# Kernel tuning notes

Hardware: AMD Instinct MI355X
Metric: run time of the kernel (lower is better)

Reference implementation:

```python
import jax, jax.numpy as jnp
import numpy as np
import math

B, C, H, W = 2, 64, 64, 64
DI = 2 * C          # d_inner
N = 16              # d_state
R = math.ceil(C / 16)  # dt_rank
K = 3               # d_conv
L = H * W

PARAM_KEYS = [
    'pe_x_w', 'pe_x_b', 'rms_x_w', 'conv_x_w', 'conv_x_b',
    'pe_info_w', 'pe_info_b', 'rms_info_w', 'conv_info_w', 'conv_info_b',
    'pe_mask_w', 'pe_mask_b', 'rms_mask_w', 'conv_mask_w', 'conv_mask_b',
    'in_x_w', 'in_info_w', 'in_mask_w',
    'delta_w', 'dt_w', 'dt_b', 'B_w', 'C_w', 'A_log', 'out_w',
]


def setup_inputs():
    key = jax.random.key(0)
    ki = iter(jax.random.split(key, 40))
    def nrm(shape, scale=1.0):
        return jax.random.normal(next(ki), shape, jnp.float32) * scale
    sc, sdi, sr, sk = 1/np.sqrt(C), 1/np.sqrt(DI), 1/np.sqrt(R), 1/np.sqrt(K)
    inp = {}
    for name in ('up', 'mask', 'x', 'y', 'z'):
        inp[name] = nrm((B, C, H, W))
    for role in ('x', 'info', 'mask'):
        inp[f'pe_{role}_w'] = nrm((3, C, C), sc)
        inp[f'pe_{role}_b'] = jnp.zeros((3, C), jnp.float32)
        inp[f'rms_{role}_w'] = jnp.ones((3, C), jnp.float32)
        inp[f'conv_{role}_w'] = nrm((3, DI, K), sk)
        inp[f'conv_{role}_b'] = nrm((3, DI), sk)
    inp['in_x_w'] = nrm((3, 2 * DI, C), sc)
    inp['in_info_w'] = nrm((3, DI, C), sc)
    inp['in_mask_w'] = nrm((3, DI, C), sc)
    inp['delta_w'] = nrm((3, R, DI), sdi)
    inp['dt_w'] = nrm((3, DI, R), sr)
    rng = np.random.default_rng(0)
    dt = np.exp(rng.uniform(size=(3, DI)) * (np.log(0.1) - np.log(0.001)) + np.log(0.001)).clip(min=1e-4)
    inp['dt_b'] = jnp.asarray(np.log(-np.expm1(-dt)), jnp.float32)
    inp['B_w'] = nrm((3, N, DI), sdi)
    inp['C_w'] = nrm((3, N, DI), sdi)
    inp['A_log'] = jnp.tile(jnp.log(jnp.arange(1, N + 1, dtype=jnp.float32)), (3, DI, 1))
    inp['out_w'] = nrm((3, C, DI), sdi)
    return inp


def embed1x1(t, w, b):
    # PatchEmbed with patch_size=1: 1x1 conv then flatten to [B, L, C]
    y = jnp.einsum('bchw,oc->bohw', t, w) + b[None, :, None, None]
    bb, cc, hh, ww = y.shape
    return y.reshape(bb, cc, hh * ww).transpose(0, 2, 1)


def rms_norm(x, w, eps=1e-5):
    return x * jax.lax.rsqrt(jnp.mean(x * x, axis=-1, keepdims=True) + eps) * w


def causal_dwconv_silu(x, w, b):
    # x [B, D, L]; depthwise causal conv1d (left-pad K-1), then SiLU
    kk = w.shape[1]
    xp = jnp.pad(x, ((0, 0), (0, 0), (kk - 1, 0)))
    y = jax.lax.conv_general_dilated(
        xp, w[:, None, :], window_strides=(1,), padding='VALID',
        dimension_numbers=('NCH', 'OIH', 'NCH'), feature_group_count=w.shape[0])
    return jax.nn.silu(y + b[None, :, None])


def selective_scan(u, delta, A, Bm, Cm):
    # u, delta: [B, D, L]; A: [D, N]; Bm, Cm: [B, N, L]
    dA = jnp.exp(jnp.einsum('bdl,dn->lbdn', delta, A))           # [L,B,D,N]
    dBu = jnp.einsum('bdl,bnl,bdl->lbdn', delta, Bm, u)          # [L,B,D,N]
    Ct = Cm.transpose(2, 0, 1)                                   # [L,B,N]
    h0 = jnp.zeros((u.shape[0], u.shape[1], A.shape[1]), u.dtype)
    def step(h, inp):
        dA_t, dBu_t, C_t = inp
        h = dA_t * h + dBu_t
        return h, jnp.einsum('bdn,bn->bd', h, C_t)
    _, ys = jax.lax.scan(step, h0, (dA, dBu, Ct))
    return ys.transpose(1, 2, 0)                                 # [B,D,L]


def branch(xin, maskin, upin, p):
    bb, cc, hh, ww = xin.shape
    xe = rms_norm(embed1x1(xin, p['pe_x_w'], p['pe_x_b']), p['rms_x_w'])        # [B,L,C]
    xz = jnp.einsum('blc,dc->bdl', xe, p['in_x_w'])                              # [B,2DI,L]
    di = xz.shape[1] // 2
    xc, x_act = xz[:, :di], xz[:, di:]
    info = rms_norm(embed1x1(upin, p['pe_info_w'], p['pe_info_b']), p['rms_info_w'])
    info = jnp.einsum('blc,dc->bdl', info, p['in_info_w'])
    mk = rms_norm(embed1x1(maskin, p['pe_mask_w'], p['pe_mask_b']), p['rms_mask_w'])
    mk = jnp.einsum('blc,dc->bdl', mk, p['in_mask_w'])
    xc = causal_dwconv_silu(xc, p['conv_x_w'], p['conv_x_b'])
    mk = causal_dwconv_silu(mk, p['conv_mask_w'], p['conv_mask_b'])
    info = causal_dwconv_silu(info, p['conv_info_w'], p['conv_info_b'])
    # S6: delta from mask, B from info, C from x
    delta = jnp.einsum('bdl,rd->brl', mk, p['delta_w'])
    delta = jnp.einsum('brl,dr->bdl', delta, p['dt_w'])
    delta = jax.nn.softplus(delta + p['dt_b'][None, :, None])
    A = -jnp.exp(p['A_log'])
    Bm = jnp.einsum('bdl,nd->bnl', info, p['B_w'])
    Cm = jnp.einsum('bdl,nd->bnl', xc, p['C_w'])
    y = selective_scan(xc, delta, A, Bm, Cm)
    y = y * jax.nn.silu(x_act)
    y = jnp.einsum('bdl,cd->blc', y, p['out_w'])
    return y.transpose(0, 2, 1).reshape(bb, cc, hh, ww) + xin


def forward(up, mask, x, y, z, *params):
    pall = dict(zip(PARAM_KEYS, params))
    out = None
    for i, feat in enumerate((x, y, z)):
        p = {k: v[i] for k, v in pall.items()}
        o = branch(feat, mask, up, p)
        out = o if out is None else out + o
    return out


def reference(up, mask, x, y, z,
              pe_x_w, pe_x_b, rms_x_w, conv_x_w, conv_x_b,
              pe_info_w, pe_info_b, rms_info_w, conv_info_w, conv_info_b,
              pe_mask_w, pe_mask_b, rms_mask_w, conv_mask_w, conv_mask_b,
              in_x_w, in_info_w, in_mask_w,
              delta_w, dt_w, dt_b, B_w, C_w, A_log, out_w):
    return forward(up, mask, x, y, z,
                   pe_x_w, pe_x_b, rms_x_w, conv_x_w, conv_x_b,
                   pe_info_w, pe_info_b, rms_info_w, conv_info_w, conv_info_b,
                   pe_mask_w, pe_mask_b, rms_mask_w, conv_mask_w, conv_mask_b,
                   in_x_w, in_info_w, in_mask_w,
                   delta_w, dt_w, dt_b, B_w, C_w, A_log, out_w)
```

## Files before the change

### kernel.cpp

```cpp
#include <hip/hip_runtime.h>
#include <math.h>

namespace {

constexpr int NB = 3;
constexpr int BB = 2;
constexpr int CC = 64;
constexpr int LLEN = 4096;
constexpr int DI = 128;
constexpr int NN = 16;
constexpr int RR = 4;
constexpr int GG = 256;
constexpr int LC = 16;
constexpr int NSEQ = NB * BB * DI * NN;
constexpr size_t SBUF = (size_t)NB * BB * DI * LLEN;

typedef _Float16 f16;
typedef __attribute__((ext_vector_type(4))) float f32x4;
typedef __attribute__((ext_vector_type(8))) short bf16x8;
typedef __attribute__((ext_vector_type(4))) _Float16 f16x4;
typedef __attribute__((ext_vector_type(8))) _Float16 f16x8;

__device__ __forceinline__ float siluf(float v) { return v / (1.f + __expf(-v)); }

__device__ __forceinline__ short cvt_bf16(float f) {
    union { float f; unsigned u; } v; v.f = f;
    unsigned r = v.u + 0x7fffu + ((v.u >> 16) & 1u);
    return (short)(r >> 16);
}
__device__ __forceinline__ unsigned pack_bf16(float lo, float hi) {
    return ((unsigned)(unsigned short)cvt_bf16(hi) << 16) | (unsigned short)cvt_bf16(lo);
}
__device__ __forceinline__ bf16x8 pack8(float4 a, float4 b) {
    bf16x8 r;
    r[0] = cvt_bf16(a.x); r[1] = cvt_bf16(a.y); r[2] = cvt_bf16(a.z); r[3] = cvt_bf16(a.w);
    r[4] = cvt_bf16(b.x); r[5] = cvt_bf16(b.y); r[6] = cvt_bf16(b.z); r[7] = cvt_bf16(b.w);
    return r;
}
__device__ __forceinline__ f16x4 to_h4(float a, float b, float c, float d) {
    f16x4 r; r[0] = (f16)a; r[1] = (f16)b; r[2] = (f16)c; r[3] = (f16)d; return r;
}
__device__ __forceinline__ float4 to_f4(f16x4 v) {
    return make_float4((float)v[0], (float)v[1], (float)v[2], (float)v[3]);
}

__global__ __launch_bounds__(256) void k1_embed(
    const float* __restrict__ up, const float* __restrict__ mask_,
    const float* __restrict__ fx, const float* __restrict__ fy, const float* __restrict__ fz,
    const float* __restrict__ pe_x_w, const float* __restrict__ pe_x_b, const float* __restrict__ rms_x_w,
    const float* __restrict__ pe_i_w, const float* __restrict__ pe_i_b, const float* __restrict__ rms_i_w,
    const float* __restrict__ pe_m_w, const float* __restrict__ pe_m_b, const float* __restrict__ rms_m_w,
    const float* __restrict__ in_x_w, const float* __restrict__ in_i_w, const float* __restrict__ in_m_w,
    f16* __restrict__ xc_pre, f16* __restrict__ x_act,
    f16* __restrict__ info_pre, f16* __restrict__ mk_pre)
{
    __shared__ short sE[64 * 64];
    __shared__ float red[4][64];
    __shared__ float sscl[64];

    int lt = blockIdx.x, job = blockIdx.y, b = blockIdx.z;
    int i = job / 3, r = job % 3;
    const float *src, *pw, *pb, *rw, *iw;
    if (r == 0) {
        src = (i == 0 ? fx : (i == 1 ? fy : fz));
        pw = pe_x_w + i * 4096; pb = pe_x_b + i * 64; rw = rms_x_w + i * 64;
        iw = in_x_w + (size_t)i * 256 * 64;
    } else if (r == 1) {
        src = up;
        pw = pe_i_w + i * 4096; pb = pe_i_b + i * 64; rw = rms_i_w + i * 64;
        iw = in_i_w + (size_t)i * 128 * 64;
    } else {
        src = mask_;
        pw = pe_m_w + i * 4096; pb = pe_m_b + i * 64; rw = rms_m_w + i * 64;
        iw = in_m_w + (size_t)i * 128 * 64;
    }
    int t = threadIdx.x;
    int w = t >> 6, lane = t & 63, lo = lane & 15, hi = lane >> 4;
    int l0 = lt * 64;
    const float* Xg = src + (size_t)b * 64 * LLEN;

    f32x4 acc1[4];
    #pragma unroll
    for (int nt = 0; nt < 4; ++nt) acc1[nt] = (f32x4){0.f, 0.f, 0.f, 0.f};

    #pragma unroll
    for (int ks = 0; ks < 2; ++ks) {
        const float* ap = pw + (16 * w + lo) * 64 + ks * 32 + hi * 8;
        bf16x8 a1 = pack8(*(const float4*)ap, *(const float4*)(ap + 4));
        #pragma unroll
        for (int nt = 0; nt < 4; ++nt) {
            const float* xc = Xg + (size_t)(ks * 32 + hi * 8) * LLEN + l0 + nt * 16 + lo;
            bf16x8 b1;
            #pragma unroll
            for (int j = 0; j < 8; ++j) b1[j] = cvt_bf16(xc[(size_t)j * LLEN]);
            acc1[nt] = __builtin_amdgcn_mfma_f32_16x16x32_bf16(a1, b1, acc1[nt], 0, 0, 0);
        }
    }

    float4 pbv = *(const float4*)&pb[16 * w + 4 * hi];
    float e_[4][4];
    #pragma unroll
    for (int nt = 0; nt < 4; ++nt) {
        e_[nt][0] = acc1[nt][0] + pbv.x;
        e_[nt][1] = acc1[nt][1] + pbv.y;
        e_[nt][2] = acc1[nt][2] + pbv.z;
        e_[nt][3] = acc1[nt][3] + pbv.w;
        float s = e_[nt][0] * e_[nt][0] + e_[nt][1] * e_[nt][1]
                + e_[nt][2] * e_[nt][2] + e_[nt][3] * e_[nt][3];
        s += __shfl_xor(s, 16);
        s += __shfl_xor(s, 32);
        if (lane < 16) red[w][nt * 16 + lo] = s;
    }
    __syncthreads();
    if (t < 64) {
        float s = red[0][t] + red[1][t] + red[2][t] + red[3][t];
        sscl[t] = rsqrtf(s * (1.f / 64.f) + 1e-5f);
    }
    __syncthreads();

    {
        int ob = 2 * w + (hi >> 1);
        #pragma unroll
        for (int nt = 0; nt < 4; ++nt) {
            float sc = sscl[16 * nt + lo];
            unsigned p0 = pack_bf16(e_[nt][0] * sc, e_[nt][1] * sc);
            unsigned p1 = pack_bf16(e_[nt][2] * sc, e_[nt][3] * sc);
            unsigned* p = (unsigned*)&sE[(16 * nt + lo) * 64 + (ob ^ (lo & 7)) * 8 + 4 * (hi & 1)];
            p[0] = p0; p[1] = p1;
        }
    }
    __syncthreads();

    bf16x8 b2[4][2];
    #pragma unroll
    for (int nt = 0; nt < 4; ++nt)
        #pragma unroll
        for (int ks = 0; ks < 2; ++ks) {
            int db = ks * 4 + hi;
            b2[nt][ks] = *(const bf16x8*)&sE[(16 * nt + lo) * 64 + (db ^ (lo & 7)) * 8];
        }

    size_t obase = ((size_t)(i * 2 + b)) * DI * LLEN;
    int MT = (r == 0) ? 4 : 2;
    for (int mm = 0; mm < MT; ++mm) {
        int m = MT * w + mm;
        bf16x8 a2[2];
        #pragma unroll
        for (int ks = 0; ks < 2; ++ks) {
            const float* wp = iw + (size_t)(16 * m + lo) * 64 + ks * 32 + hi * 8;
            float4 w0 = *(const float4*)wp;
            float4 w1 = *(const float4*)(wp + 4);
            float4 r0 = *(const float4*)&rw[ks * 32 + hi * 8];
            float4 r1 = *(const float4*)&rw[ks * 32 + hi * 8 + 4];
            w0.x *= r0.x; w0.y *= r0.y; w0.z *= r0.z; w0.w *= r0.w;
            w1.x *= r1.x; w1.y *= r1.y; w1.z *= r1.z; w1.w *= r1.w;
            a2[ks] = pack8(w0, w1);
        }
        f32x4 acc2[4];
        #pragma unroll
        for (int nt = 0; nt < 4; ++nt) acc2[nt] = (f32x4){0.f, 0.f, 0.f, 0.f};
        #pragma unroll
        for (int ks = 0; ks < 2; ++ks)
            #pragma unroll
            for (int nt = 0; nt < 4; ++nt)
                acc2[nt] = __builtin_amdgcn_mfma_f32_16x16x32_bf16(a2[ks], b2[nt][ks], acc2[nt], 0, 0, 0);

        int d0 = 16 * m + 4 * hi;
        f16* dst; int dd = d0;
        if (r == 0) { if (d0 < 128) dst = xc_pre; else { dst = x_act; dd = d0 - 128; } }
        else if (r == 1) dst = info_pre;
        else dst = mk_pre;
        #pragma unroll
        for (int nt = 0; nt < 4; ++nt) {
            int l = l0 + 16 * nt + lo;
            *(f16x4*)&dst[obase + (size_t)l * DI + dd] =
                to_h4(acc2[nt][0], acc2[nt][1], acc2[nt][2], acc2[nt][3]);
        }
    }
}

__global__ __launch_bounds__(256) void k3_conv(
    const f16* __restrict__ xc_pre, const f16* __restrict__ info_pre, const f16* __restrict__ mk_pre,
    const float* __restrict__ conv_x_w, const float* __restrict__ conv_x_b,
    const float* __restrict__ conv_i_w, const float* __restrict__ conv_i_b,
    const float* __restrict__ conv_m_w, const float* __restrict__ conv_m_b,
    const float* __restrict__ delta_w, const float* __restrict__ dt_w, const float* __restrict__ dt_b,
    const float* __restrict__ B_w, const float* __restrict__ C_w,
    f16* __restrict__ u, f16* __restrict__ delta,
    f16* __restrict__ Bm, f16* __restrict__ Cm)
{
    __shared__ __align__(16) float ot[64 * 128];
    __shared__ float rvec[4 * 64];

    int lt = blockIdx.x, ib = blockIdx.y, strm = blockIdx.z;
    int i = ib >> 1;
    int t = threadIdx.x;
    int l0 = lt * 64;
    size_t base = (size_t)ib * DI * LLEN;

    const f16 *inb; const float *cw, *cb;
    if (strm == 0)      { inb = mk_pre;   cw = conv_m_w + i * DI * 3; cb = conv_m_b + i * DI; }
    else if (strm == 1) { inb = info_pre; cw = conv_i_w + i * DI * 3; cb = conv_i_b + i * DI; }
    else                { inb = xc_pre;   cw = conv_x_w + i * DI * 3; cb = conv_x_b + i * DI; }

    {
        int d4 = t & 31, lq = t >> 5;
        int d = d4 * 4;
        float cw0[4], cw1[4], cw2[4], cbb[4];
        #pragma unroll
        for (int j = 0; j < 4; ++j) {
            cw0[j] = cw[(d + j) * 3 + 0];
            cw1[j] = cw[(d + j) * 3 + 1];
            cw2[j] = cw[(d + j) * 3 + 2];
            cbb[j] = cb[d + j];
        }
        int gl0 = l0 + lq * 8;
        float4 x0 = make_float4(0.f, 0.f, 0.f, 0.f), x1 = x0;
        if (gl0 >= 2) x0 = to_f4(*(const f16x4*)&inb[base + (size_t)(gl0 - 2) * DI + d]);
        if (gl0 >= 1) x1 = to_f4(*(const f16x4*)&inb[base + (size_t)(gl0 - 1) * DI + d]);
        #pragma unroll
        for (int li = 0; li < 8; ++li) {
            int l = lq * 8 + li;
            float4 x2 = to_f4(*(const f16x4*)&inb[base + (size_t)(gl0 + li) * DI + d]);
            float4 v;
            v.x = siluf(cw0[0] * x0.x + cw1[0] * x1.x + cw2[0] * x2.x + cbb[0]);
            v.y = siluf(cw0[1] * x0.y + cw1[1] * x1.y + cw2[1] * x2.y + cbb[1]);
            v.z = siluf(cw0[2] * x0.z + cw1[2] * x1.z + cw2[2] * x2.z + cbb[2]);
            v.w = siluf(cw0[3] * x0.w + cw1[3] * x1.w + cw2[3] * x2.w + cbb[3]);
            *(float4*)&ot[l * 128 + ((d4 * 4) ^ ((l & 7) << 2))] = v;
            if (strm == 2) *(f16x4*)&u[base + (size_t)(gl0 + li) * DI + d] = to_h4(v.x, v.y, v.z, v.w);
            x0 = x1; x1 = x2;
        }
    }
    __syncthreads();

    if (strm == 0) {
        {
            int l = t & 63, r = t >> 6, sw = (l & 7) << 2;
            const float* dw = delta_w + i * RR * DI + r * DI;
            float acc = 0.f;
            #pragma unroll
            for (int d4 = 0; d4 < 32; ++d4) {
                float4 v = *(const float4*)&ot[l * 128 + ((d4 * 4) ^ sw)];
                int db = d4 * 4;
                acc += dw[db] * v.x + dw[db + 1] * v.y + dw[db + 2] * v.z + dw[db + 3] * v.w;
            }
            rvec[r * 64 + l] = acc;
        }
        __syncthreads();
        {
            int d = t & 127, lh = t >> 7;
            const float* dtw = dt_w + i * DI * RR + d * RR;
            float w0 = dtw[0], w1 = dtw[1], w2 = dtw[2], w3 = dtw[3];
            float bb = dt_b[i * DI + d];
            #pragma unroll 4
            for (int li = 0; li < 32; ++li) {
                int l = lh * 32 + li;
                float v = bb + w0 * rvec[l] + w1 * rvec[64 + l] + w2 * rvec[128 + l] + w3 * rvec[192 + l];
                float sp = (v > 20.f) ? v : log1pf(__expf(v));
                delta[base + (size_t)(l0 + l) * DI + d] = (f16)sp;
            }
        }
    } else {
        int l = t & 63, ng = t >> 6, sw = (l & 7) << 2;
        const float* wv = ((strm == 1) ? B_w : C_w) + i * NN * DI + ng * 4 * DI;
        float a0 = 0.f, a1 = 0.f, a2 = 0.f, a3 = 0.f;
        #pragma unroll
        for (int d4 = 0; d4 < 32; ++d4) {
            float4 v = *(const float4*)&ot[l * 128 + ((d4 * 4) ^ sw)];
            int db = d4 * 4;
            a0 += wv[db] * v.x + wv[db + 1] * v.y + wv[db + 2] * v.z + wv[db + 3] * v.w;
            a1 += wv[DI + db] * v.x + wv[DI + db + 1] * v.y + wv[DI + db + 2] * v.z + wv[DI + db + 3] * v.w;
            a2 += wv[2 * DI + db] * v.x + wv[2 * DI + db + 1] * v.y + wv[2 * DI + db + 2] * v.z + wv[2 * DI + db + 3] * v.w;
            a3 += wv[3 * DI + db] * v.x + wv[3 * DI + db + 1] * v.y + wv[3 * DI + db + 2] * v.z + wv[3 * DI + db + 3] * v.w;
        }
        f16* dst = (strm == 1) ? Bm : Cm;
        *(f16x4*)&dst[((size_t)ib * LLEN + l0 + l) * NN + ng * 4] = to_h4(a0, a1, a2, a3);
    }
}

__global__ __launch_bounds__(128) void k4_scan1(
    const f16* __restrict__ u, const f16* __restrict__ delta,
    const f16* __restrict__ Bm, const float* __restrict__ A_log,
    f16* __restrict__ aprod, f16* __restrict__ hend)
{
    __shared__ __align__(16) float sB[LC * 16];
    int g = blockIdx.x, ib = blockIdx.y, i = ib >> 1;
    int d = threadIdx.x;
    if (d < 64) {
        f16x4 v = ((const f16x4*)(Bm + ((size_t)ib * LLEN + (size_t)g * LC) * NN))[d];
        ((float4*)sB)[d] = to_f4(v);
    }
    float A[16], h[16];
    {
        const float4* al = (const float4*)(A_log + ((size_t)i * DI + d) * NN);
        #pragma unroll
        for (int q = 0; q < 4; ++q) {
            float4 v = al[q];
            A[4 * q] = -__expf(v.x); A[4 * q + 1] = -__expf(v.y);
            A[4 * q + 2] = -__expf(v.z); A[4 * q + 3] = -__expf(v.w);
        }
    }
    #pragma unroll
    for (int n = 0; n < 16; ++n) h[n] = 0.f;
    float sdl = 0.f;
    __syncthreads();
    size_t base = ((size_t)ib * LLEN + (size_t)g * LC) * DI + d;
    #pragma unroll 4
    for (int li = 0; li < LC; ++li) {
        float dl = (float)delta[base + li * DI];
        float du = dl * (float)u[base + li * DI];
        sdl += dl;
        const float4* bl = (const float4*)(sB + li * 16);
        float4 b0 = bl[0], b1 = bl[1], b2 = bl[2], b3 = bl[3];
        h[0] = __expf(dl * A[0]) * h[0] + du * b0.x;  h[1] = __expf(dl * A[1]) * h[1] + du * b0.y;
        h[2] = __expf(dl * A[2]) * h[2] + du * b0.z;  h[3] = __expf(dl * A[3]) * h[3] + du * b0.w;
        h[4] = __expf(dl * A[4]) * h[4] + du * b1.x;  h[5] = __expf(dl * A[5]) * h[5] + du * b1.y;
        h[6] = __expf(dl * A[6]) * h[6] + du * b1.z;  h[7] = __expf(dl * A[7]) * h[7] + du * b1.w;
        h[8] = __expf(dl * A[8]) * h[8] + du * b2.x;  h[9] = __expf(dl * A[9]) * h[9] + du * b2.y;
        h[10] = __expf(dl * A[10]) * h[10] + du * b2.z; h[11] = __expf(dl * A[11]) * h[11] + du * b2.w;
        h[12] = __expf(dl * A[12]) * h[12] + du * b3.x; h[13] = __expf(dl * A[13]) * h[13] + du * b3.y;
        h[14] = __expf(dl * A[14]) * h[14] + du * b3.z; h[15] = __expf(dl * A[15]) * h[15] + du * b3.w;
    }
    size_t seq = ((size_t)ib * DI + d) * NN;
    f16x8* ap = (f16x8*)(aprod + (size_t)g * NSEQ + seq);
    f16x8* he = (f16x8*)(hend + (size_t)g * NSEQ + seq);
    #pragma unroll
    for (int q = 0; q < 2; ++q) {
        f16x8 av, hv;
        #pragma unroll
        for (int j = 0; j < 8; ++j) {
            av[j] = (f16)__expf(A[8 * q + j] * sdl);
            hv[j] = (f16)h[8 * q + j];
        }
        ap[q] = av; he[q] = hv;
    }
}

__global__ __launch_bounds__(256) void k5_prefix(
    const f16* __restrict__ aprod, const f16* __restrict__ hend,
    f16* __restrict__ hin)
{
    int s = blockIdx.x * 256 + threadIdx.x;
    float h = 0.f;
    #pragma unroll 8
    for (int g = 0; g < GG; ++g) {
        hin[(size_t)g * NSEQ + s] = (f16)h;
        h = (float)aprod[(size_t)g * NSEQ + s] * h + (float)hend[(size_t)g * NSEQ + s];
    }
}

__global__ __launch_bounds__(128) void k6_scan2(
    const f16* __restrict__ u, const f16* __restrict__ delta,
    const f16* __restrict__ Bm, const f16* __restrict__ Cm,
    const float* __restrict__ A_log, const f16* __restrict__ hin,
    f16* __restrict__ y)
{
    __shared__ __align__(16) float sB[LC * 16];
    __shared__ __align__(16) float sC[LC * 16];
    int g = blockIdx.x, ib = blockIdx.y, i = ib >> 1;
    int d = threadIdx.x;
    {
        const f16x4* bsrc = (const f16x4*)(Bm + ((size_t)ib * LLEN + (size_t)g * LC) * NN);
        const f16x4* csrc = (const f16x4*)(Cm + ((size_t)ib * LLEN + (size_t)g * LC) * NN);
        if (d < 64) ((float4*)sB)[d] = to_f4(bsrc[d]);
        else ((float4*)sC)[d - 64] = to_f4(csrc[d - 64]);
    }
    float A[16], h[16];
    {
        const float4* al = (const float4*)(A_log + ((size_t)i * DI + d) * NN);
        #pragma unroll
        for (int q = 0; q < 4; ++q) {
            float4 v = al[q];
            A[4 * q] = -__expf(v.x); A[4 * q + 1] = -__expf(v.y);
            A[4 * q + 2] = -__expf(v.z); A[4 * q + 3] = -__expf(v.w);
        }
    }
    {
        size_t seq = ((size_t)ib * DI + d) * NN;
        const f16x8* hp = (const f16x8*)(hin + (size_t)g * NSEQ + seq);
        #pragma unroll
        for (int q = 0; q < 2; ++q) {
            f16x8 v = hp[q];
            #pragma unroll
            for (int j = 0; j < 8; ++j) h[8 * q + j] = (float)v[j];
        }
    }
    __syncthreads();
    size_t base = ((size_t)ib * LLEN + (size_t)g * LC) * DI + d;
    #pragma unroll 4
    for (int li = 0; li < LC; ++li) {
        float dl = (float)delta[base + li * DI];
        float du = dl * (float)u[base + li * DI];
        const float4* bl = (const float4*)(sB + li * 16);
        const float4* cl = (const float4*)(sC + li * 16);
        float4 b0 = bl[0], b1 = bl[1], b2 = bl[2], b3 = bl[3];
        float4 c0 = cl[0], c1 = cl[1], c2 = cl[2], c3 = cl[3];
        float acc = 0.f;
        h[0] = __expf(dl * A[0]) * h[0] + du * b0.x;  acc += h[0] * c0.x;
        h[1] = __expf(dl * A[1]) * h[1] + du * b0.y;  acc += h[1] * c0.y;
        h[2] = __expf(dl * A[2]) * h[2] + du * b0.z;  acc += h[2] * c0.z;
        h[3] = __expf(dl * A[3]) * h[3] + du * b0.w;  acc += h[3] * c0.w;
        h[4] = __expf(dl * A[4]) * h[4] + du * b1.x;  acc += h[4] * c1.x;
        h[5] = __expf(dl * A[5]) * h[5] + du * b1.y;  acc += h[5] * c1.y;
        h[6] = __expf(dl * A[6]) * h[6] + du * b1.z;  acc += h[6] * c1.z;
        h[7] = __expf(dl * A[7]) * h[7] + du * b1.w;  acc += h[7] * c1.w;
        h[8] = __expf(dl * A[8]) * h[8] + du * b2.x;  acc += h[8] * c2.x;
        h[9] = __expf(dl * A[9]) * h[9] + du * b2.y;  acc += h[9] * c2.y;
        h[10] = __expf(dl * A[10]) * h[10] + du * b2.z; acc += h[10] * c2.z;
        h[11] = __expf(dl * A[11]) * h[11] + du * b2.w; acc += h[11] * c2.w;
        h[12] = __expf(dl * A[12]) * h[12] + du * b3.x; acc += h[12] * c3.x;
        h[13] = __expf(dl * A[13]) * h[13] + du * b3.y; acc += h[13] * c3.y;
        h[14] = __expf(dl * A[14]) * h[14] + du * b3.z; acc += h[14] * c3.z;
        h[15] = __expf(dl * A[15]) * h[15] + du * b3.w; acc += h[15] * c3.w;
        y[base + li * DI] = (f16)acc;
    }
}

__global__ __launch_bounds__(256) void k7_out(
    const f16* __restrict__ y, const f16* __restrict__ xact,
    const float* __restrict__ out_w,
    const float* __restrict__ fx, const float* __restrict__ fy, const float* __restrict__ fz,
    float* __restrict__ out)
{
    __shared__ short sG[64 * 128];
    int lt = blockIdx.x, b = blockIdx.y;
    int l0 = lt * 64;
    int t = threadIdx.x;
    int w = t >> 6, lane = t & 63, lo = lane & 15, hi = lane >> 4;

    f32x4 acc[4];
    #pragma unroll
    for (int nt = 0; nt < 4; ++nt) acc[nt] = (f32x4){0.f, 0.f, 0.f, 0.f};

    for (int i = 0; i < 3; ++i) {
        size_t base = ((size_t)(i * 2 + b)) * DI * LLEN;
        __syncthreads();
        #pragma unroll
        for (int p = 0; p < 8; ++p) {
            int idx = t + 256 * p;
            int d4 = idx & 31, l = idx >> 5;
            int d = d4 * 4;
            float4 yv = to_f4(*(const f16x4*)&y[base + (size_t)(l0 + l) * DI + d]);
            float4 xa = to_f4(*(const f16x4*)&xact[base + (size_t)(l0 + l) * DI + d]);
            float g0 = yv.x * siluf(xa.x), g1 = yv.y * siluf(xa.y);
            float g2 = yv.z * siluf(xa.z), g3 = yv.w * siluf(xa.w);
            int blk = d4 >> 1;
            int blks = (blk & 8) | ((blk ^ (l & 7)) & 7);
            unsigned* p32 = (unsigned*)&sG[l * 128 + blks * 8 + 4 * (d4 & 1)];
            p32[0] = pack_bf16(g0, g1);
            p32[1] = pack_bf16(g2, g3);
        }
        __syncthreads();

        const float* ow = out_w + (size_t)i * CC * DI;
        bf16x8 a[4];
        #pragma unroll
        for (int ks = 0; ks < 4; ++ks) {
            const float* ap = ow + (size_t)(16 * w + lo) * 128 + ks * 32 + hi * 8;
            a[ks] = pack8(*(const float4*)ap, *(const float4*)(ap + 4));
        }
        #pragma unroll
        for (int nt = 0; nt < 4; ++nt) {
            int l = 16 * nt + lo;
            #pragma unroll
            for (int ks = 0; ks < 4; ++ks) {
                int db = ks * 4 + hi;
                int blks = (db & 8) | ((db ^ (l & 7)) & 7);
                bf16x8 bv = *(const bf16x8*)&sG[l * 128 + blks * 8];
                acc[nt] = __builtin_amdgcn_mfma_f32_16x16x32_bf16(a[ks], bv, acc[nt], 0, 0, 0);
            }
        }
    }

    #pragma unroll
    for (int nt = 0; nt < 4; ++nt) {
        int l = l0 + 16 * nt + lo;
        int cbase = 16 * w + 4 * hi;
        #pragma unroll
        for (int rr = 0; rr < 4; ++rr) {
            int c = cbase + rr;
            size_t idx = ((size_t)b * CC + c) * LLEN + l;
            out[idx] = acc[nt][rr] + fx[idx] + fy[idx] + fz[idx];
        }
    }
}

}

extern "C" void kernel_launch(void* const* d_in, const int* in_sizes, int n_in,
                              void* d_out, int out_size, void* d_ws, size_t ws_size,
                              hipStream_t stream)
{
    (void)in_sizes; (void)n_in; (void)out_size; (void)ws_size;
    const float* up       = (const float*)d_in[0];
    const float* mask_    = (const float*)d_in[1];
    const float* fx       = (const float*)d_in[2];
    const float* fy       = (const float*)d_in[3];
    const float* fz       = (const float*)d_in[4];
    const float* pe_x_w   = (const float*)d_in[5];
    const float* pe_x_b   = (const float*)d_in[6];
    const float* rms_x_w  = (const float*)d_in[7];
    const float* conv_x_w = (const float*)d_in[8];
    const float* conv_x_b = (const float*)d_in[9];
    const float* pe_i_w   = (const float*)d_in[10];
    const float* pe_i_b   = (const float*)d_in[11];
    const float* rms_i_w  = (const float*)d_in[12];
    const float* conv_i_w = (const float*)d_in[13];
    const float* conv_i_b = (const float*)d_in[14];
    const float* pe_m_w   = (const float*)d_in[15];
    const float* pe_m_b   = (const float*)d_in[16];
    const float* rms_m_w  = (const float*)d_in[17];
    const float* conv_m_w = (const float*)d_in[18];
    const float* conv_m_b = (const float*)d_in[19];
    const float* in_x_w   = (const float*)d_in[20];
    const float* in_i_w   = (const float*)d_in[21];
    const float* in_m_w   = (const float*)d_in[22];
    const float* delta_w  = (const float*)d_in[23];
    const float* dt_w     = (const float*)d_in[24];
    const float* dt_b     = (const float*)d_in[25];
    const float* B_w      = (const float*)d_in[26];
    const float* C_w      = (const float*)d_in[27];
    const float* A_log    = (const float*)d_in[28];
    const float* out_w    = (const float*)d_in[29];
    float* out = (float*)d_out;

    f16* ws = (f16*)d_ws;
    const size_t S = SBUF;
    f16* xc_pre   = ws;
    f16* x_act    = ws + S;
    f16* info_pre = ws + 2 * S;
    f16* mk_pre   = ws + 3 * S;
    f16* ubuf     = ws + 4 * S;
    f16* dbuf     = ws + 5 * S;
    f16* BmB      = ws + 6 * S;
    f16* CmB      = BmB + (size_t)NB * BB * NN * LLEN;
    f16* aprod = info_pre;
    f16* hendb = mk_pre;
    f16* hinb  = xc_pre;
    f16* ybuf  = info_pre;

    hipLaunchKernelGGL(k1_embed, dim3(64, 9, 2), dim3(256), 0, stream,
        up, mask_, fx, fy, fz,
        pe_x_w, pe_x_b, rms_x_w, pe_i_w, pe_i_b, rms_i_w, pe_m_w, pe_m_b, rms_m_w,
        in_x_w, in_i_w, in_m_w, xc_pre, x_act, info_pre, mk_pre);

    hipLaunchKernelGGL(k3_conv, dim3(64, 6, 3), dim3(256), 0, stream,
        xc_pre, info_pre, mk_pre,
        conv_x_w, conv_x_b, conv_i_w, conv_i_b, conv_m_w, conv_m_b,
        delta_w, dt_w, dt_b, B_w, C_w, ubuf, dbuf, BmB, CmB);

    hipLaunchKernelGGL(k4_scan1, dim3(GG, 6), dim3(128), 0, stream,
        ubuf, dbuf, BmB, A_log, aprod, hendb);

    hipLaunchKernelGGL(k5_prefix, dim3(NSEQ / 256), dim3(256), 0, stream,
        aprod, hendb, hinb);

    hipLaunchKernelGGL(k6_scan2, dim3(GG, 6), dim3(128), 0, stream,
        ubuf, dbuf, BmB, CmB, A_log, hinb, ybuf);

    hipLaunchKernelGGL(k7_out, dim3(64, 2), dim3(256), 0, stream,
        ybuf, x_act, out_w, fx, fy, fz, out);
}
```

Measured before the change: 133.0 us.

## Fuse conv, projections and first scan pass; move gating into second scan

The three-stream conv kernel becomes one kernel per chunk. It computes the mask, info and x convolutions in sequence and keeps the results in f16 shared memory. It then runs the chunk-local first scan pass in place, so the separate scan1 kernel and its reloads of u, delta and Bm are gone. The chunk count is halved and the chunk length doubled. The second scan now applies the SiLU(x_act) gate and writes bf16 directly, so the output kernel just copies tiles into shared memory. In exchange each fused block does more serial work, there are fewer blocks, and aprod/hend need extra workspace beyond the previous buffers.

Result: slower. 146.1 us (+9.8%).

```diff
diff --git a/kernel.cpp b/kernel.cpp
--- a/kernel.cpp
+++ b/kernel.cpp
@@ -10,8 +10,8 @@
 constexpr int DI = 128;
 constexpr int NN = 16;
 constexpr int RR = 4;
-constexpr int GG = 256;
-constexpr int LC = 16;
+constexpr int GG = 128;
+constexpr int LC = 32;
 constexpr int NSEQ = NB * BB * DI * NN;
 constexpr size_t SBUF = (size_t)NB * BB * DI * LLEN;
 
@@ -42,6 +42,11 @@
 }
 __device__ __forceinline__ float4 to_f4(f16x4 v) {
     return make_float4((float)v[0], (float)v[1], (float)v[2], (float)v[3]);
+}
+__device__ __forceinline__ int swz16(int l, int d) {
+    int b = d >> 3;
+    int bs = (b & 8) | ((b ^ l) & 7);
+    return l * 128 + bs * 8 + (d & 7);
 }
 
 __global__ __launch_bounds__(256) void k1_embed(
@@ -186,24 +191,25 @@
     const float* __restrict__ conv_m_w, const float* __restrict__ conv_m_b,
     const float* __restrict__ delta_w, const float* __restrict__ dt_w, const float* __restrict__ dt_b,
     const float* __restrict__ B_w, const float* __restrict__ C_w,
+    const float* __restrict__ A_log,
     f16* __restrict__ u, f16* __restrict__ delta,
-    f16* __restrict__ Bm, f16* __restrict__ Cm)
+    f16* __restrict__ Bm, f16* __restrict__ Cm,
+    f16* __restrict__ aprod, f16* __restrict__ hend)
 {
-    __shared__ __align__(16) float ot[64 * 128];
-    __shared__ float rvec[4 * 64];
-
-    int lt = blockIdx.x, ib = blockIdx.y, strm = blockIdx.z;
+    __shared__ __align__(16) f16 ot[LC * 128];
+    __shared__ __align__(16) f16 sdelH[LC * 128];
+    __shared__ __align__(16) f16 otU[LC * 128];
+    __shared__ __align__(16) float sB[LC * 16];
+    __shared__ float rvec[4 * LC];
+
+    int g = blockIdx.x, ib = blockIdx.y;
     int i = ib >> 1;
-    int t = threadIdx.x;
-    int l0 = lt * 64;
+    int t = threadIdx.x, lane = t & 63;
+    int l0 = g * LC;
     size_t base = (size_t)ib * DI * LLEN;
 
-    const f16 *inb; const float *cw, *cb;
-    if (strm == 0)      { inb = mk_pre;   cw = conv_m_w + i * DI * 3; cb = conv_m_b + i * DI; }
-    else if (strm == 1) { inb = info_pre; cw = conv_i_w + i * DI * 3; cb = conv_i_b + i * DI; }
-    else                { inb = xc_pre;   cw = conv_x_w + i * DI * 3; cb = conv_x_b + i * DI; }
-
-    {
+    auto conv_stream = [&](const f16* inb, const float* cw, const float* cb,
+                           f16* lds, bool store_u) {
         int d4 = t & 31, lq = t >> 5;
         int d = d4 * 4;
         float cw0[4], cw1[4], cw2[4], cbb[4];
@@ -214,126 +220,146 @@
             cw2[j] = cw[(d + j) * 3 + 2];
             cbb[j] = cb[d + j];
         }
-        int gl0 = l0 + lq * 8;
+        int gl0 = l0 + lq * 4;
         float4 x0 = make_float4(0.f, 0.f, 0.f, 0.f), x1 = x0;
         if (gl0 >= 2) x0 = to_f4(*(const f16x4*)&inb[base + (size_t)(gl0 - 2) * DI + d]);
         if (gl0 >= 1) x1 = to_f4(*(const f16x4*)&inb[base + (size_t)(gl0 - 1) * DI + d]);
         #pragma unroll
-        for (int li = 0; li < 8; ++li) {
-            int l = lq * 8 + li;
+        for (int li = 0; li < 4; ++li) {
+            int l = lq * 4 + li;
             float4 x2 = to_f4(*(const f16x4*)&inb[base + (size_t)(gl0 + li) * DI + d]);
             float4 v;
             v.x = siluf(cw0[0] * x0.x + cw1[0] * x1.x + cw2[0] * x2.x + cbb[0]);
             v.y = siluf(cw0[1] * x0.y + cw1[1] * x1.y + cw2[1] * x2.y + cbb[1]);
             v.z = siluf(cw0[2] * x0.z + cw1[2] * x1.z + cw2[2] * x2.z + cbb[2]);
             v.w = siluf(cw0[3] * x0.w + cw1[3] * x1.w + cw2[3] * x2.w + cbb[3]);
-            *(float4*)&ot[l * 128 + ((d4 * 4) ^ ((l & 7) << 2))] = v;
-            if (strm == 2) *(f16x4*)&u[base + (size_t)(gl0 + li) * DI + d] = to_h4(v.x, v.y, v.z, v.w);
+            f16x4 hv = to_h4(v.x, v.y, v.z, v.w);
+            *(f16x4*)&lds[swz16(l, d)] = hv;
+            if (store_u) *(f16x4*)&u[base + (size_t)(gl0 + li) * DI + d] = hv;
             x0 = x1; x1 = x2;
         }
-    }
-    __syncthreads();
-
-    if (strm == 0) {
-        {
-            int l = t & 63, r = t >> 6, sw = (l & 7) << 2;
-            const float* dw = delta_w + i * RR * DI + r * DI;
-            float acc = 0.f;
+    };
+
+    conv_stream(mk_pre, conv_m_w + i * DI * 3, conv_m_b + i * DI, ot, false);
+    __syncthreads();
+    {
+        int l = t & 31, r = t >> 6;
+        const float* dw = delta_w + i * RR * DI + r * DI;
+        float acc = 0.f;
+        #pragma unroll
+        for (int db = 0; db < 16; ++db) {
+            f16x8 v = *(const f16x8*)&ot[swz16(l, db * 8)];
+            int d0 = db * 8;
+            acc += dw[d0] * (float)v[0] + dw[d0 + 1] * (float)v[1]
+                 + dw[d0 + 2] * (float)v[2] + dw[d0 + 3] * (float)v[3]
+                 + dw[d0 + 4] * (float)v[4] + dw[d0 + 5] * (float)v[5]
+                 + dw[d0 + 6] * (float)v[6] + dw[d0 + 7] * (float)v[7];
+        }
+        if (lane < 32) rvec[r * LC + l] = acc;
+    }
+    __syncthreads();
+    {
+        int d = t & 127, lh = t >> 7;
+        const float* dtw = dt_w + i * DI * RR + d * RR;
+        float w0 = dtw[0], w1 = dtw[1], w2 = dtw[2], w3 = dtw[3];
+        float bb = dt_b[i * DI + d];
+        #pragma unroll
+        for (int li = 0; li < 16; ++li) {
+            int l = lh * 16 + li;
+            float v = bb + w0 * rvec[l] + w1 * rvec[LC + l] + w2 * rvec[2 * LC + l] + w3 * rvec[3 * LC + l];
+            float sp = (v > 20.f) ? v : log1pf(__expf(v));
+            f16 h = (f16)sp;
+            delta[base + (size_t)(l0 + l) * DI + d] = h;
+            sdelH[swz16(l, d)] = h;
+        }
+    }
+    __syncthreads();
+    conv_stream(info_pre, conv_i_w + i * DI * 3, conv_i_b + i * DI, ot, false);
+    __syncthreads();
+    {
+        int l = t & 31, w = t >> 6;
+        const float* bw = B_w + i * NN * DI + (w * 4) * DI;
+        float a0 = 0.f, a1 = 0.f, a2 = 0.f, a3 = 0.f;
+        #pragma unroll
+        for (int db = 0; db < 16; ++db) {
+            f16x8 v = *(const f16x8*)&ot[swz16(l, db * 8)];
+            int d0 = db * 8;
             #pragma unroll
-            for (int d4 = 0; d4 < 32; ++d4) {
-                float4 v = *(const float4*)&ot[l * 128 + ((d4 * 4) ^ sw)];
-                int db = d4 * 4;
-                acc += dw[db] * v.x + dw[db + 1] * v.y + dw[db + 2] * v.z + dw[db + 3] * v.w;
+            for (int j = 0; j < 8; ++j) {
+                float x = (float)v[j];
+                a0 += bw[d0 + j] * x;
+                a1 += bw[DI + d0 + j] * x;
+                a2 += bw[2 * DI + d0 + j] * x;
+                a3 += bw[3 * DI + d0 + j] * x;
             }
-            rvec[r * 64 + l] = acc;
-        }
-        __syncthreads();
-        {
-            int d = t & 127, lh = t >> 7;
-            const float* dtw = dt_w + i * DI * RR + d * RR;
-            float w0 = dtw[0], w1 = dtw[1], w2 = dtw[2], w3 = dtw[3];
-            float bb = dt_b[i * DI + d];
-            #pragma unroll 4
-            for (int li = 0; li < 32; ++li) {
-                int l = lh * 32 + li;
-                float v = bb + w0 * rvec[l] + w1 * rvec[64 + l] + w2 * rvec[128 + l] + w3 * rvec[192 + l];
-                float sp = (v > 20.f) ? v : log1pf(__expf(v));
-                delta[base + (size_t)(l0 + l) * DI + d] = (f16)sp;
+        }
+        if (lane < 32) {
+            *(f16x4*)&Bm[((size_t)ib * LLEN + l0 + l) * NN + w * 4] = to_h4(a0, a1, a2, a3);
+            sB[l * 16 + w * 4 + 0] = a0; sB[l * 16 + w * 4 + 1] = a1;
+            sB[l * 16 + w * 4 + 2] = a2; sB[l * 16 + w * 4 + 3] = a3;
+        }
+    }
+    conv_stream(xc_pre, conv_x_w + i * DI * 3, conv_x_b + i * DI, otU, true);
+    __syncthreads();
+    {
+        int l = t & 31, w = t >> 6;
+        const float* cwv = C_w + i * NN * DI + (w * 4) * DI;
+        float a0 = 0.f, a1 = 0.f, a2 = 0.f, a3 = 0.f;
+        #pragma unroll
+        for (int db = 0; db < 16; ++db) {
+            f16x8 v = *(const f16x8*)&otU[swz16(l, db * 8)];
+            int d0 = db * 8;
+            #pragma unroll
+            for (int j = 0; j < 8; ++j) {
+                float x = (float)v[j];
+                a0 += cwv[d0 + j] * x;
+                a1 += cwv[DI + d0 + j] * x;
+                a2 += cwv[2 * DI + d0 + j] * x;
+                a3 += cwv[3 * DI + d0 + j] * x;
             }
         }
-    } else {
-        int l = t & 63, ng = t >> 6, sw = (l & 7) << 2;
-        const float* wv = ((strm == 1) ? B_w : C_w) + i * NN * DI + ng * 4 * DI;
-        float a0 = 0.f, a1 = 0.f, a2 = 0.f, a3 = 0.f;
-        #pragma unroll
-        for (int d4 = 0; d4 < 32; ++d4) {
-            float4 v = *(const float4*)&ot[l * 128 + ((d4 * 4) ^ sw)];
-            int db = d4 * 4;
-            a0 += wv[db] * v.x + wv[db + 1] * v.y + wv[db + 2] * v.z + wv[db + 3] * v.w;
-            a1 += wv[DI + db] * v.x + wv[DI + db + 1] * v.y + wv[DI + db + 2] * v.z + wv[DI + db + 3] * v.w;
-            a2 += wv[2 * DI + db] * v.x + wv[2 * DI + db + 1] * v.y + wv[2 * DI + db + 2] * v.z + wv[2 * DI + db + 3] * v.w;
-            a3 += wv[3 * DI + db] * v.x + wv[3 * DI + db + 1] * v.y + wv[3 * DI + db + 2] * v.z + wv[3 * DI + db + 3] * v.w;
-        }
-        f16* dst = (strm == 1) ? Bm : Cm;
-        *(f16x4*)&dst[((size_t)ib * LLEN + l0 + l) * NN + ng * 4] = to_h4(a0, a1, a2, a3);
-    }
-}
-
-__global__ __launch_bounds__(128) void k4_scan1(
-    const f16* __restrict__ u, const f16* __restrict__ delta,
-    const f16* __restrict__ Bm, const float* __restrict__ A_log,
-    f16* __restrict__ aprod, f16* __restrict__ hend)
-{
-    __shared__ __align__(16) float sB[LC * 16];
-    int g = blockIdx.x, ib = blockIdx.y, i = ib >> 1;
-    int d = threadIdx.x;
-    if (d < 64) {
-        f16x4 v = ((const f16x4*)(Bm + ((size_t)ib * LLEN + (size_t)g * LC) * NN))[d];
-        ((float4*)sB)[d] = to_f4(v);
-    }
-    float A[16], h[16];
-    {
-        const float4* al = (const float4*)(A_log + ((size_t)i * DI + d) * NN);
-        #pragma unroll
-        for (int q = 0; q < 4; ++q) {
+        if (lane < 32)
+            *(f16x4*)&Cm[((size_t)ib * LLEN + l0 + l) * NN + w * 4] = to_h4(a0, a1, a2, a3);
+    }
+    {
+        int d = t & 127, ng = t >> 7;
+        float A[8], h[8];
+        const float4* al = (const float4*)(A_log + ((size_t)i * DI + d) * NN + ng * 8);
+        #pragma unroll
+        for (int q = 0; q < 2; ++q) {
             float4 v = al[q];
             A[4 * q] = -__expf(v.x); A[4 * q + 1] = -__expf(v.y);
             A[4 * q + 2] = -__expf(v.z); A[4 * q + 3] = -__expf(v.w);
         }
-    }
-    #pragma unroll
-    for (int n = 0; n < 16; ++n) h[n] = 0.f;
-    float sdl = 0.f;
-    __syncthreads();
-    size_t base = ((size_t)ib * LLEN + (size_t)g * LC) * DI + d;
-    #pragma unroll 4
-    for (int li = 0; li < LC; ++li) {
-        float dl = (float)delta[base + li * DI];
-        float du = dl * (float)u[base + li * DI];
-        sdl += dl;
-        const float4* bl = (const float4*)(sB + li * 16);
-        float4 b0 = bl[0], b1 = bl[1], b2 = bl[2], b3 = bl[3];
-        h[0] = __expf(dl * A[0]) * h[0] + du * b0.x;  h[1] = __expf(dl * A[1]) * h[1] + du * b0.y;
-        h[2] = __expf(dl * A[2]) * h[2] + du * b0.z;  h[3] = __expf(dl * A[3]) * h[3] + du * b0.w;
-        h[4] = __expf(dl * A[4]) * h[4] + du * b1.x;  h[5] = __expf(dl * A[5]) * h[5] + du * b1.y;
-        h[6] = __expf(dl * A[6]) * h[6] + du * b1.z;  h[7] = __expf(dl * A[7]) * h[7] + du * b1.w;
-        h[8] = __expf(dl * A[8]) * h[8] + du * b2.x;  h[9] = __expf(dl * A[9]) * h[9] + du * b2.y;
-        h[10] = __expf(dl * A[10]) * h[10] + du * b2.z; h[11] = __expf(dl * A[11]) * h[11] + du * b2.w;
-        h[12] = __expf(dl * A[12]) * h[12] + du * b3.x; h[13] = __expf(dl * A[13]) * h[13] + du * b3.y;
-        h[14] = __expf(dl * A[14]) * h[14] + du * b3.z; h[15] = __expf(dl * A[15]) * h[15] + du * b3.w;
-    }
-    size_t seq = ((size_t)ib * DI + d) * NN;
-    f16x8* ap = (f16x8*)(aprod + (size_t)g * NSEQ + seq);
-    f16x8* he = (f16x8*)(hend + (size_t)g * NSEQ + seq);
-    #pragma unroll
-    for (int q = 0; q < 2; ++q) {
+        #pragma unroll
+        for (int n = 0; n < 8; ++n) h[n] = 0.f;
+        float sdl = 0.f;
+        #pragma unroll 4
+        for (int li = 0; li < LC; ++li) {
+            float dl = (float)sdelH[swz16(li, d)];
+            float uu = (float)otU[swz16(li, d)];
+            float du = dl * uu;
+            sdl += dl;
+            float4 b0 = *(const float4*)&sB[li * 16 + ng * 8];
+            float4 b1 = *(const float4*)&sB[li * 16 + ng * 8 + 4];
+            h[0] = __expf(dl * A[0]) * h[0] + du * b0.x;
+            h[1] = __expf(dl * A[1]) * h[1] + du * b0.y;
+            h[2] = __expf(dl * A[2]) * h[2] + du * b0.z;
+            h[3] = __expf(dl * A[3]) * h[3] + du * b0.w;
+            h[4] = __expf(dl * A[4]) * h[4] + du * b1.x;
+            h[5] = __expf(dl * A[5]) * h[5] + du * b1.y;
+            h[6] = __expf(dl * A[6]) * h[6] + du * b1.z;
+            h[7] = __expf(dl * A[7]) * h[7] + du * b1.w;
+        }
+        size_t seq = ((size_t)ib * DI + d) * NN + ng * 8;
         f16x8 av, hv;
         #pragma unroll
         for (int j = 0; j < 8; ++j) {
-            av[j] = (f16)__expf(A[8 * q + j] * sdl);
-            hv[j] = (f16)h[8 * q + j];
-        }
-        ap[q] = av; he[q] = hv;
+            av[j] = (f16)__expf(A[j] * sdl);
+            hv[j] = (f16)h[j];
+        }
+        *(f16x8*)&aprod[(size_t)g * NSEQ + seq] = av;
+        *(f16x8*)&hend[(size_t)g * NSEQ + seq] = hv;
     }
 }
 
@@ -354,7 +380,8 @@
     const f16* __restrict__ u, const f16* __restrict__ delta,
     const f16* __restrict__ Bm, const f16* __restrict__ Cm,
     const float* __restrict__ A_log, const f16* __restrict__ hin,
-    f16* __restrict__ y)
+    const f16* __restrict__ xact,
+    short* __restrict__ G)
 {
     __shared__ __align__(16) float sB[LC * 16];
     __shared__ __align__(16) float sC[LC * 16];
@@ -363,8 +390,8 @@
     {
         const f16x4* bsrc = (const f16x4*)(Bm + ((size_t)ib * LLEN + (size_t)g * LC) * NN);
         const f16x4* csrc = (const f16x4*)(Cm + ((size_t)ib * LLEN + (size_t)g * LC) * NN);
-        if (d < 64) ((float4*)sB)[d] = to_f4(bsrc[d]);
-        else ((float4*)sC)[d - 64] = to_f4(csrc[d - 64]);
+        ((float4*)sB)[d] = to_f4(bsrc[d]);
+        ((float4*)sC)[d] = to_f4(csrc[d]);
     }
     float A[16], h[16];
     {
@@ -413,12 +440,13 @@
         h[13] = __expf(dl * A[13]) * h[13] + du * b3.y; acc += h[13] * c3.y;
         h[14] = __expf(dl * A[14]) * h[14] + du * b3.z; acc += h[14] * c3.z;
         h[15] = __expf(dl * A[15]) * h[15] + du * b3.w; acc += h[15] * c3.w;
-        y[base + li * DI] = (f16)acc;
+        float xa = (float)xact[base + li * DI];
+        G[base + li * DI] = cvt_bf16(acc * siluf(xa));
     }
 }
 
 __global__ __launch_bounds__(256) void k7_out(
-    const f16* __restrict__ y, const f16* __restrict__ xact,
+    const short* __restrict__ G,
     const float* __restrict__ out_w,
     const float* __restrict__ fx, const float* __restrict__ fy, const float* __restrict__ fz,
     float* __restrict__ out)
@@ -437,19 +465,12 @@
         size_t base = ((size_t)(i * 2 + b)) * DI * LLEN;
         __syncthreads();
         #pragma unroll
-        for (int p = 0; p < 8; ++p) {
+        for (int p = 0; p < 4; ++p) {
             int idx = t + 256 * p;
-            int d4 = idx & 31, l = idx >> 5;
-            int d = d4 * 4;
-            float4 yv = to_f4(*(const f16x4*)&y[base + (size_t)(l0 + l) * DI + d]);
-            float4 xa = to_f4(*(const f16x4*)&xact[base + (size_t)(l0 + l) * DI + d]);
-            float g0 = yv.x * siluf(xa.x), g1 = yv.y * siluf(xa.y);
-            float g2 = yv.z * siluf(xa.z), g3 = yv.w * siluf(xa.w);
-            int blk = d4 >> 1;
-            int blks = (blk & 8) | ((blk ^ (l & 7)) & 7);
-            unsigned* p32 = (unsigned*)&sG[l * 128 + blks * 8 + 4 * (d4 & 1)];
-            p32[0] = pack_bf16(g0, g1);
-            p32[1] = pack_bf16(g2, g3);
+            int db = idx & 15, l = idx >> 4;
+            bf16x8 v = *(const bf16x8*)&G[base + (size_t)(l0 + l) * DI + db * 8];
+            int bs = (db & 8) | ((db ^ (l & 7)) & 7);
+            *(bf16x8*)&sG[l * 128 + bs * 8] = v;
         }
         __syncthreads();
 
@@ -466,8 +487,8 @@
             #pragma unroll
             for (int ks = 0; ks < 4; ++ks) {
                 int db = ks * 4 + hi;
-                int blks = (db & 8) | ((db ^ (l & 7)) & 7);
-                bf16x8 bv = *(const bf16x8*)&sG[l * 128 + blks * 8];
+                int bs = (db & 8) | ((db ^ (l & 7)) & 7);
+                bf16x8 bv = *(const bf16x8*)&sG[l * 128 + bs * 8];
                 acc[nt] = __builtin_amdgcn_mfma_f32_16x16x32_bf16(a[ks], bv, acc[nt], 0, 0, 0);
             }
         }
@@ -535,30 +556,28 @@
     f16* dbuf     = ws + 5 * S;
     f16* BmB      = ws + 6 * S;
     f16* CmB      = BmB + (size_t)NB * BB * NN * LLEN;
-    f16* aprod = info_pre;
-    f16* hendb = mk_pre;
+    f16* aprodb   = CmB + (size_t)NB * BB * NN * LLEN;
+    f16* hendb    = aprodb + (size_t)GG * NSEQ;
     f16* hinb  = xc_pre;
-    f16* ybuf  = info_pre;
+    short* Gbuf = (short*)info_pre;
 
     hipLaunchKernelGGL(k1_embed, dim3(64, 9, 2), dim3(256), 0, stream,
         up, mask_, fx, fy, fz,
         pe_x_w, pe_x_b, rms_x_w, pe_i_w, pe_i_b, rms_i_w, pe_m_w, pe_m_b, rms_m_w,
         in_x_w, in_i_w, in_m_w, xc_pre, x_act, info_pre, mk_pre);
 
-    hipLaunchKernelGGL(k3_conv, dim3(64, 6, 3), dim3(256), 0, stream,
+    hipLaunchKernelGGL(k3_conv, dim3(GG, 6), dim3(256), 0, stream,
         xc_pre, info_pre, mk_pre,
         conv_x_w, conv_x_b, conv_i_w, conv_i_b, conv_m_w, conv_m_b,
-        delta_w, dt_w, dt_b, B_w, C_w, ubuf, dbuf, BmB, CmB);
-
-    hipLaunchKernelGGL(k4_scan1, dim3(GG, 6), dim3(128), 0, stream,
-        ubuf, dbuf, BmB, A_log, aprod, hendb);
+        delta_w, dt_w, dt_b, B_w, C_w, A_log,
+        ubuf, dbuf, BmB, CmB, aprodb, hendb);
 
     hipLaunchKernelGGL(k5_prefix, dim3(NSEQ / 256), dim3(256), 0, stream,
-        aprod, hendb, hinb);
+        aprodb, hendb, hinb);
 
     hipLaunchKernelGGL(k6_scan2, dim3(GG, 6), dim3(128), 0, stream,
-        ubuf, dbuf, BmB, CmB, A_log, hinb, ybuf);
+        ubuf, dbuf, BmB, CmB, A_log, hinb, x_act, Gbuf);
 
     hipLaunchKernelGGL(k7_out, dim3(64, 2), dim3(256), 0, stream,
-        ybuf, x_act, out_w, fx, fy, fz, out);
-}
+        Gbuf, out_w, fx, fy, fz, out);
+}
```
